# Performance work log

Measured on AMD Instinct MI355X. Metric: run time of the kernel, lower is better.

Reference implementation:

```python
import jax, jax.numpy as jnp
import numpy as np

EMBED_DIM = 512
EDGE_COUNT = 200
BATCH = 1024
N_SBJ = 1      # subject entities per example
N_OBJ = 64     # candidate object entities per example


def setup_inputs() -> dict:
    key = jax.random.key(0)
    k1, k2, k3, k4 = jax.random.split(key, 4)
    sbj_embs = jax.random.normal(k1, (BATCH, N_SBJ, EMBED_DIM), dtype=jnp.float32)
    obj_embs = jax.random.normal(k2, (BATCH, N_OBJ, EMBED_DIM), dtype=jnp.float32)
    rel_ids = jax.random.randint(k3, (BATCH,), 0, EDGE_COUNT, dtype=jnp.int64)
    # W_r initialized as diagonal matrices from uniform values (as in __init__),
    # but stored as full dense [edge_count, d, d] trainable tensor.
    diag_vals = jax.random.uniform(k4, (EDGE_COUNT, EMBED_DIM), dtype=jnp.float32)
    W_r = jax.vmap(jnp.diag)(diag_vals)  # [edge_count, d, d]
    return {"sbj_embs": sbj_embs, "obj_embs": obj_embs, "rel_ids": rel_ids, "W_r": W_r}


def reference(sbj_embs, obj_embs, rel_ids, W_r):
    # rel_embs: gather per-relation dense matrix  [B, d, d]
    rel_embs = W_r[rel_ids]
    # sbj_rel = sbj @ rel : [B, n, d]
    sbj_rel = jnp.einsum('bnd,bde->bne', sbj_embs, rel_embs)
    # scores = sbj_rel @ obj^T : [B, n, m], then sum over n -> [B, m]
    scores = jnp.einsum('bne,bme->bm', sbj_rel, obj_embs)
    return scores
```

## Files before the change

### kernel.cpp

```cpp
#include <hip/hip_runtime.h>


#define D      512
#define NOBJ   64

__global__ __launch_bounds__(256) void decoder_kernel(
    const float* __restrict__ sbj,
    const float* __restrict__ obj,
    const int*   __restrict__ rel,
    const float* __restrict__ Wr,
    float*       __restrict__ out)
{
    const int b = blockIdx.x;
    const int t = threadIdx.x;

    __shared__ float s_lds[D];
    __shared__ float v_lds[D];

    {
        const float2 sv = reinterpret_cast<const float2*>(sbj + (size_t)b * D)[t];
        s_lds[2 * t]     = sv.x;
        s_lds[2 * t + 1] = sv.y;
    }
    __syncthreads();

    const float2* __restrict__ W2 =
        reinterpret_cast<const float2*>(Wr + (size_t)rel[b] * D * D);

    float acc0 = 0.f, acc1 = 0.f;
    #pragma unroll 8
    for (int d = 0; d < D; ++d) {
        const float  sd = s_lds[d];
        const float2 w  = W2[d * (D / 2) + t];
        acc0 = fmaf(sd, w.x, acc0);
        acc1 = fmaf(sd, w.y, acc1);
    }
    v_lds[2 * t]     = acc0;
    v_lds[2 * t + 1] = acc1;
    __syncthreads();

    const int wave = t >> 6;
    const int lane = t & 63;

    float vreg[8];
    #pragma unroll
    for (int k = 0; k < 8; ++k) vreg[k] = v_lds[lane * 8 + k];

    const float* __restrict__ objb = obj + (size_t)b * NOBJ * D;

    #pragma unroll 4
    for (int j = 0; j < 16; ++j) {
        const int m = wave * 16 + j;
        const float4* __restrict__ o4 =
            reinterpret_cast<const float4*>(objb + (size_t)m * D);
        const float4 a = o4[lane * 2];
        const float4 c = o4[lane * 2 + 1];

        float p = vreg[0] * a.x + vreg[1] * a.y + vreg[2] * a.z + vreg[3] * a.w
                + vreg[4] * c.x + vreg[5] * c.y + vreg[6] * c.z + vreg[7] * c.w;

        #pragma unroll
        for (int off = 32; off > 0; off >>= 1)
            p += __shfl_down(p, off, 64);

        if (lane == 0) out[(size_t)b * NOBJ + m] = p;
    }
}

extern "C" void kernel_launch(void* const* d_in, const int* in_sizes, int n_in,
                              void* d_out, int out_size, void* d_ws, size_t ws_size,
                              hipStream_t stream) {
    const float* sbj = (const float*)d_in[0];
    const float* obj = (const float*)d_in[1];
    const int*   rel = (const int*)d_in[2];
    const float* Wr  = (const float*)d_in[3];
    float*       out = (float*)d_out;

    const int B = in_sizes[2];
    decoder_kernel<<<dim3(B), dim3(256), 0, stream>>>(sbj, obj, rel, Wr, out);
}
```

Baseline: 416.6 us.

## Group batch items by relation to reuse W_r reads across a chunk

Adds a prep kernel that bucket-sorts batch indices by relation id and splits each bucket into chunks of up to 8. A GEMV kernel then streams each relation's dense 512x512 matrix once per chunk and multiplies it against all subject vectors in that chunk, writing intermediate vectors to workspace. A separate score kernel dots those vectors with the object embeddings. This cuts redundant W_r traffic, which dominates the original per-example kernel, at the cost of two extra launches, a single-block serial prep step and a workspace round trip. It falls back to the fused kernel when the workspace is too small.

```diff
diff --git a/kernel.cpp b/kernel.cpp
--- a/kernel.cpp
+++ b/kernel.cpp
@@ -1,68 +1,199 @@
 #include <hip/hip_runtime.h>
 
 
-#define D      512
-#define NOBJ   64
-
-__global__ __launch_bounds__(256) void decoder_kernel(
-    const float* __restrict__ sbj,
-    const float* __restrict__ obj,
-    const int*   __restrict__ rel,
-    const float* __restrict__ Wr,
-    float*       __restrict__ out)
+#define D        512
+#define NOBJ     64
+#define EDGES    200
+#define G        8
+
+__device__ __forceinline__ float4 f4zero() { float4 z; z.x=z.y=z.z=z.w=0.f; return z; }
+
+__global__ __launch_bounds__(256) void prep_kernel(
+    const int* __restrict__ rel, int B,
+    int* __restrict__ sorted, int* __restrict__ chunk_rel,
+    int* __restrict__ chunk_start, int* __restrict__ chunk_cnt,
+    int* __restrict__ nchunks)
+{
+    __shared__ int cnt[EDGES];
+    __shared__ int off[EDGES];
+    __shared__ int pos[EDGES];
+    __shared__ int nch;
+    const int t = threadIdx.x;
+
+    if (t < EDGES) cnt[t] = 0;
+    if (t == 0) nch = 0;
+    __syncthreads();
+
+    for (int b = t; b < B; b += 256) atomicAdd(&cnt[rel[b]], 1);
+    __syncthreads();
+
+    if (t == 0) {
+        int a = 0;
+        for (int r = 0; r < EDGES; ++r) { off[r] = a; a += cnt[r]; }
+    }
+    if (t < EDGES) pos[t] = 0;
+    __syncthreads();
+
+    for (int b = t; b < B; b += 256) {
+        const int r = rel[b];
+        const int p = atomicAdd(&pos[r], 1);
+        sorted[off[r] + p] = b;
+    }
+
+    if (t < EDGES) {
+        const int n = cnt[t];
+        if (n > 0) {
+            const int nc   = (n + G - 1) / G;
+            const int base = atomicAdd(&nch, nc);
+            for (int k = 0; k < nc; ++k) {
+                chunk_rel[base + k]   = t;
+                chunk_start[base + k] = off[t] + k * G;
+                chunk_cnt[base + k]   = min(G, n - k * G);
+            }
+        }
+    }
+    __syncthreads();
+    if (t == 0) *nchunks = nch;
+}
+
+__global__ __launch_bounds__(256) void gemv_kernel(
+    const float* __restrict__ sbj, const float* __restrict__ Wr,
+    const int* __restrict__ sorted,
+    const int* __restrict__ chunk_rel, const int* __restrict__ chunk_start,
+    const int* __restrict__ chunk_cnt, const int* __restrict__ nchunks,
+    float* __restrict__ V)
+{
+    const int cid = blockIdx.x >> 1;
+    if (cid >= *nchunks) return;
+    const int colbase = (blockIdx.x & 1) * 256;
+    const int t    = threadIdx.x;
+    const int lane = t & 63;
+    const int wv   = t >> 6;
+
+    __shared__ float lds[8192];
+
+    const int relid = chunk_rel[cid];
+    const int start = chunk_start[cid];
+    const int cnt   = chunk_cnt[cid];
+
+    #pragma unroll
+    for (int g = 0; g < G; ++g) {
+        float2 v2;
+        if (g < cnt) {
+            v2 = reinterpret_cast<const float2*>(sbj + (size_t)sorted[start + g] * D)[t];
+        } else { v2.x = 0.f; v2.y = 0.f; }
+        lds[g * D + 2 * t]     = v2.x;
+        lds[g * D + 2 * t + 1] = v2.y;
+    }
+    __syncthreads();
+
+    const float4* __restrict__ W4 =
+        reinterpret_cast<const float4*>(Wr) + (size_t)relid * (D * D / 4) + (colbase >> 2) + lane;
+
+    float4 acc[G];
+    #pragma unroll
+    for (int g = 0; g < G; ++g) acc[g] = f4zero();
+
+    #pragma unroll 4
+    for (int d4 = 0; d4 < D; d4 += 4) {
+        const int d = d4 + wv;
+        const float4 w = W4[(size_t)d * (D / 4)];
+        #pragma unroll
+        for (int g = 0; g < G; ++g) {
+            const float sg = lds[g * D + d];
+            acc[g].x = fmaf(sg, w.x, acc[g].x);
+            acc[g].y = fmaf(sg, w.y, acc[g].y);
+            acc[g].z = fmaf(sg, w.z, acc[g].z);
+            acc[g].w = fmaf(sg, w.w, acc[g].w);
+        }
+    }
+    __syncthreads();
+
+    #pragma unroll
+    for (int g = 0; g < G; ++g)
+        reinterpret_cast<float4*>(lds)[(wv * G + g) * 64 + lane] = acc[g];
+    __syncthreads();
+
+    for (int g = 0; g < cnt; ++g) {
+        const float s = lds[(0 * G + g) * 256 + t] + lds[(1 * G + g) * 256 + t]
+                      + lds[(2 * G + g) * 256 + t] + lds[(3 * G + g) * 256 + t];
+        V[(size_t)sorted[start + g] * D + colbase + t] = s;
+    }
+}
+
+__global__ __launch_bounds__(256) void score_kernel(
+    const float* __restrict__ V, const float* __restrict__ obj,
+    float* __restrict__ out)
+{
+    const int b    = blockIdx.x;
+    const int t    = threadIdx.x;
+    const int lane = t & 63;
+    const int wv   = t >> 6;
+
+    const float4* __restrict__ v4 = reinterpret_cast<const float4*>(V + (size_t)b * D);
+    const float4 a = v4[lane * 2];
+    const float4 c = v4[lane * 2 + 1];
+    float vreg[8] = {a.x, a.y, a.z, a.w, c.x, c.y, c.z, c.w};
+
+    const float* __restrict__ objb = obj + (size_t)b * NOBJ * D;
+
+    #pragma unroll 4
+    for (int j = 0; j < 16; ++j) {
+        const int m = wv * 16 + j;
+        const float4* __restrict__ o4 = reinterpret_cast<const float4*>(objb + (size_t)m * D);
+        const float4 x = o4[lane * 2];
+        const float4 y = o4[lane * 2 + 1];
+
+        float p = vreg[0] * x.x + vreg[1] * x.y + vreg[2] * x.z + vreg[3] * x.w
+                + vreg[4] * y.x + vreg[5] * y.y + vreg[6] * y.z + vreg[7] * y.w;
+
+        #pragma unroll
+        for (int off = 32; off > 0; off >>= 1)
+            p += __shfl_down(p, off, 64);
+
+        if (lane == 0) out[(size_t)b * NOBJ + m] = p;
+    }
+}
+
+__global__ __launch_bounds__(256) void fused_kernel(
+    const float* __restrict__ sbj, const float* __restrict__ obj,
+    const int* __restrict__ rel, const float* __restrict__ Wr,
+    float* __restrict__ out)
 {
     const int b = blockIdx.x;
     const int t = threadIdx.x;
-
     __shared__ float s_lds[D];
     __shared__ float v_lds[D];
-
     {
         const float2 sv = reinterpret_cast<const float2*>(sbj + (size_t)b * D)[t];
-        s_lds[2 * t]     = sv.x;
-        s_lds[2 * t + 1] = sv.y;
-    }
-    __syncthreads();
-
-    const float2* __restrict__ W2 =
-        reinterpret_cast<const float2*>(Wr + (size_t)rel[b] * D * D);
-
+        s_lds[2 * t] = sv.x; s_lds[2 * t + 1] = sv.y;
+    }
+    __syncthreads();
+    const float2* __restrict__ W2 = reinterpret_cast<const float2*>(Wr + (size_t)rel[b] * D * D);
     float acc0 = 0.f, acc1 = 0.f;
     #pragma unroll 8
     for (int d = 0; d < D; ++d) {
-        const float  sd = s_lds[d];
-        const float2 w  = W2[d * (D / 2) + t];
-        acc0 = fmaf(sd, w.x, acc0);
-        acc1 = fmaf(sd, w.y, acc1);
-    }
-    v_lds[2 * t]     = acc0;
-    v_lds[2 * t + 1] = acc1;
-    __syncthreads();
-
-    const int wave = t >> 6;
-    const int lane = t & 63;
-
+        const float sd = s_lds[d];
+        const float2 w = W2[d * (D / 2) + t];
+        acc0 = fmaf(sd, w.x, acc0); acc1 = fmaf(sd, w.y, acc1);
+    }
+    v_lds[2 * t] = acc0; v_lds[2 * t + 1] = acc1;
+    __syncthreads();
+    const int wave = t >> 6, lane = t & 63;
     float vreg[8];
     #pragma unroll
     for (int k = 0; k < 8; ++k) vreg[k] = v_lds[lane * 8 + k];
-
     const float* __restrict__ objb = obj + (size_t)b * NOBJ * D;
-
     #pragma unroll 4
     for (int j = 0; j < 16; ++j) {
         const int m = wave * 16 + j;
-        const float4* __restrict__ o4 =
-            reinterpret_cast<const float4*>(objb + (size_t)m * D);
+        const float4* __restrict__ o4 = reinterpret_cast<const float4*>(objb + (size_t)m * D);
         const float4 a = o4[lane * 2];
         const float4 c = o4[lane * 2 + 1];
-
-        float p = vreg[0] * a.x + vreg[1] * a.y + vreg[2] * a.z + vreg[3] * a.w
-                + vreg[4] * c.x + vreg[5] * c.y + vreg[6] * c.z + vreg[7] * c.w;
-
+        float p = vreg[0]*a.x + vreg[1]*a.y + vreg[2]*a.z + vreg[3]*a.w
+                + vreg[4]*c.x + vreg[5]*c.y + vreg[6]*c.z + vreg[7]*c.w;
         #pragma unroll
-        for (int off = 32; off > 0; off >>= 1)
-            p += __shfl_down(p, off, 64);
-
+        for (int off = 32; off > 0; off >>= 1) p += __shfl_down(p, off, 64);
         if (lane == 0) out[(size_t)b * NOBJ + m] = p;
     }
 }
@@ -75,7 +206,35 @@
     const int*   rel = (const int*)d_in[2];
     const float* Wr  = (const float*)d_in[3];
     float*       out = (float*)d_out;
-
     const int B = in_sizes[2];
-    decoder_kernel<<<dim3(B), dim3(256), 0, stream>>>(sbj, obj, rel, Wr, out);
-}
+
+    const int maxch = B / G + EDGES;
+
+    const size_t offV      = 0;
+    const size_t offSorted = (size_t)B * D * 4;
+    const size_t offCRel   = offSorted + (size_t)B * 4;
+    const size_t offCStart = offCRel   + (size_t)maxch * 4;
+    const size_t offCCnt   = offCStart + (size_t)maxch * 4;
+    const size_t offNCh    = offCCnt   + (size_t)maxch * 4;
+    const size_t needed    = offNCh + 64;
+
+    if (ws_size < needed) {
+        fused_kernel<<<dim3(B), dim3(256), 0, stream>>>(sbj, obj, rel, Wr, out);
+        return;
+    }
+
+    char* ws = (char*)d_ws;
+    float* V          = (float*)(ws + offV);
+    int*   sorted     = (int*)(ws + offSorted);
+    int*   chunk_rel  = (int*)(ws + offCRel);
+    int*   chunk_start= (int*)(ws + offCStart);
+    int*   chunk_cnt  = (int*)(ws + offCCnt);
+    int*   nchunks    = (int*)(ws + offNCh);
+
+    prep_kernel<<<dim3(1), dim3(256), 0, stream>>>(rel, B, sorted, chunk_rel,
+                                                   chunk_start, chunk_cnt, nchunks);
+    gemv_kernel<<<dim3(2 * maxch), dim3(256), 0, stream>>>(sbj, Wr, sorted,
+                                                           chunk_rel, chunk_start,
+                                                           chunk_cnt, nchunks, V);
+    score_kernel<<<dim3(B), dim3(256), 0, stream>>>(V, obj, out);
+}
```

Result: faster. 382.8 us (-8.1%).

## Sort batch by relation and map same-relation blocks to one XCD for L2 reuse

Applied to the files above, without the earlier changes.

Adds a single-block prep kernel that counting-sorts batch indices by relation id into workspace. The main kernel remaps block ids so that consecutive sorted examples land on the same XCD, letting blocks that share a W_r matrix reuse it from that XCD's L2 instead of refetching the 1 MB matrix from HBM. The W-times-s product is also restructured into two halves of d using float4 loads, reduced through LDS. This costs an extra serial launch and a single-block sort, and the original kernel is kept as a fallback when workspace is too small.

```diff
diff --git a/kernel.cpp b/kernel.cpp
--- a/kernel.cpp
+++ b/kernel.cpp
@@ -3,19 +3,60 @@
 
 #define D      512
 #define NOBJ   64
+#define EDGES  200
 
-__global__ __launch_bounds__(256) void decoder_kernel(
-    const float* __restrict__ sbj,
-    const float* __restrict__ obj,
-    const int*   __restrict__ rel,
-    const float* __restrict__ Wr,
-    float*       __restrict__ out)
+__global__ __launch_bounds__(256) void prep_kernel(
+    const int* __restrict__ rel, int B, int* __restrict__ sorted)
 {
-    const int b = blockIdx.x;
+    __shared__ int cnt[256];
+    __shared__ int scan[256];
+    __shared__ int off[256];
+    __shared__ int pos[256];
     const int t = threadIdx.x;
 
+    cnt[t] = 0; pos[t] = 0;
+    __syncthreads();
+
+    for (int b = t; b < B; b += 256) atomicAdd(&cnt[rel[b]], 1);
+    __syncthreads();
+
+    int val = cnt[t];
+    scan[t] = val;
+    __syncthreads();
+    for (int o = 1; o < 256; o <<= 1) {
+        int v = (t >= o) ? scan[t - o] : 0;
+        __syncthreads();
+        scan[t] += v;
+        __syncthreads();
+    }
+    off[t] = scan[t] - val;
+    __syncthreads();
+
+    for (int b = t; b < B; b += 256) {
+        const int r = rel[b];
+        sorted[off[r] + atomicAdd(&pos[r], 1)] = b;
+    }
+}
+
+__global__ __launch_bounds__(256) void main_kernel(
+    const float* __restrict__ sbj, const float* __restrict__ obj,
+    const float* __restrict__ Wr,  const int* __restrict__ rel,
+    const int* __restrict__ sorted, float* __restrict__ out)
+{
+    int wg;
+    {
+        const int nwg = gridDim.x;
+        const int q = nwg >> 3, r = nwg & 7;
+        const int xcd = blockIdx.x & 7, idx = blockIdx.x >> 3;
+        wg = (xcd < r ? xcd * (q + 1) : r * (q + 1) + (xcd - r) * q) + idx;
+    }
+    const int b    = sorted[wg];
+    const int t    = threadIdx.x;
+    const int lane = t & 63;
+    const int wv   = t >> 6;
+
     __shared__ float s_lds[D];
-    __shared__ float v_lds[D];
+    __shared__ float p_lds[2 * D];
 
     {
         const float2 sv = reinterpret_cast<const float2*>(sbj + (size_t)b * D)[t];
@@ -24,33 +65,53 @@
     }
     __syncthreads();
 
-    const float2* __restrict__ W2 =
-        reinterpret_cast<const float2*>(Wr + (size_t)rel[b] * D * D);
+    const int c4 = (t & 127) << 2;
+    const int h  = t >> 7;
 
-    float acc0 = 0.f, acc1 = 0.f;
-    #pragma unroll 8
-    for (int d = 0; d < D; ++d) {
-        const float  sd = s_lds[d];
-        const float2 w  = W2[d * (D / 2) + t];
-        acc0 = fmaf(sd, w.x, acc0);
-        acc1 = fmaf(sd, w.y, acc1);
+    const float4* __restrict__ W4 =
+        reinterpret_cast<const float4*>(Wr + (size_t)rel[b] * D * D)
+        + (size_t)(h * 256) * (D / 4) + (c4 >> 2);
+    const float* __restrict__ sp = s_lds + h * 256;
+
+    float4 acc; acc.x = acc.y = acc.z = acc.w = 0.f;
+
+    #pragma unroll 4
+    for (int d4 = 0; d4 < 256; d4 += 4) {
+        const float4 sd4 = *reinterpret_cast<const float4*>(sp + d4);
+        const float4 w0 = W4[(size_t)(d4 + 0) * (D / 4)];
+        const float4 w1 = W4[(size_t)(d4 + 1) * (D / 4)];
+        const float4 w2 = W4[(size_t)(d4 + 2) * (D / 4)];
+        const float4 w3 = W4[(size_t)(d4 + 3) * (D / 4)];
+        acc.x = fmaf(sd4.x, w0.x, acc.x); acc.y = fmaf(sd4.x, w0.y, acc.y);
+        acc.z = fmaf(sd4.x, w0.z, acc.z); acc.w = fmaf(sd4.x, w0.w, acc.w);
+        acc.x = fmaf(sd4.y, w1.x, acc.x); acc.y = fmaf(sd4.y, w1.y, acc.y);
+        acc.z = fmaf(sd4.y, w1.z, acc.z); acc.w = fmaf(sd4.y, w1.w, acc.w);
+        acc.x = fmaf(sd4.z, w2.x, acc.x); acc.y = fmaf(sd4.z, w2.y, acc.y);
+        acc.z = fmaf(sd4.z, w2.z, acc.z); acc.w = fmaf(sd4.z, w2.w, acc.w);
+        acc.x = fmaf(sd4.w, w3.x, acc.x); acc.y = fmaf(sd4.w, w3.y, acc.y);
+        acc.z = fmaf(sd4.w, w3.z, acc.z); acc.w = fmaf(sd4.w, w3.w, acc.w);
     }
-    v_lds[2 * t]     = acc0;
-    v_lds[2 * t + 1] = acc1;
+
+    reinterpret_cast<float4*>(p_lds)[h * 128 + (c4 >> 2)] = acc;
     __syncthreads();
 
-    const int wave = t >> 6;
-    const int lane = t & 63;
+    {
+        const float2 pa = *reinterpret_cast<const float2*>(p_lds + 2 * t);
+        const float2 pb = *reinterpret_cast<const float2*>(p_lds + D + 2 * t);
+        s_lds[2 * t]     = pa.x + pb.x;
+        s_lds[2 * t + 1] = pa.y + pb.y;
+    }
+    __syncthreads();
 
     float vreg[8];
     #pragma unroll
-    for (int k = 0; k < 8; ++k) vreg[k] = v_lds[lane * 8 + k];
+    for (int k = 0; k < 8; ++k) vreg[k] = s_lds[lane * 8 + k];
 
     const float* __restrict__ objb = obj + (size_t)b * NOBJ * D;
 
     #pragma unroll 4
     for (int j = 0; j < 16; ++j) {
-        const int m = wave * 16 + j;
+        const int m = wv * 16 + j;
         const float4* __restrict__ o4 =
             reinterpret_cast<const float4*>(objb + (size_t)m * D);
         const float4 a = o4[lane * 2];
@@ -67,6 +128,49 @@
     }
 }
 
+__global__ __launch_bounds__(256) void fused_kernel(
+    const float* __restrict__ sbj, const float* __restrict__ obj,
+    const int* __restrict__ rel, const float* __restrict__ Wr,
+    float* __restrict__ out)
+{
+    const int b = blockIdx.x;
+    const int t = threadIdx.x;
+    __shared__ float s_lds[D];
+    __shared__ float v_lds[D];
+    {
+        const float2 sv = reinterpret_cast<const float2*>(sbj + (size_t)b * D)[t];
+        s_lds[2 * t] = sv.x; s_lds[2 * t + 1] = sv.y;
+    }
+    __syncthreads();
+    const float2* __restrict__ W2 = reinterpret_cast<const float2*>(Wr + (size_t)rel[b] * D * D);
+    float acc0 = 0.f, acc1 = 0.f;
+    #pragma unroll 8
+    for (int d = 0; d < D; ++d) {
+        const float sd = s_lds[d];
+        const float2 w = W2[d * (D / 2) + t];
+        acc0 = fmaf(sd, w.x, acc0); acc1 = fmaf(sd, w.y, acc1);
+    }
+    v_lds[2 * t] = acc0; v_lds[2 * t + 1] = acc1;
+    __syncthreads();
+    const int wave = t >> 6, lane = t & 63;
+    float vreg[8];
+    #pragma unroll
+    for (int k = 0; k < 8; ++k) vreg[k] = v_lds[lane * 8 + k];
+    const float* __restrict__ objb = obj + (size_t)b * NOBJ * D;
+    #pragma unroll 4
+    for (int j = 0; j < 16; ++j) {
+        const int mm = wave * 16 + j;
+        const float4* __restrict__ o4 = reinterpret_cast<const float4*>(objb + (size_t)mm * D);
+        const float4 a = o4[lane * 2];
+        const float4 c = o4[lane * 2 + 1];
+        float p = vreg[0]*a.x + vreg[1]*a.y + vreg[2]*a.z + vreg[3]*a.w
+                + vreg[4]*c.x + vreg[5]*c.y + vreg[6]*c.z + vreg[7]*c.w;
+        #pragma unroll
+        for (int off = 32; off > 0; off >>= 1) p += __shfl_down(p, off, 64);
+        if (lane == 0) out[(size_t)b * NOBJ + mm] = p;
+    }
+}
+
 extern "C" void kernel_launch(void* const* d_in, const int* in_sizes, int n_in,
                               void* d_out, int out_size, void* d_ws, size_t ws_size,
                               hipStream_t stream) {
@@ -75,7 +179,14 @@
     const int*   rel = (const int*)d_in[2];
     const float* Wr  = (const float*)d_in[3];
     float*       out = (float*)d_out;
+    const int B = in_sizes[2];
 
-    const int B = in_sizes[2];
-    decoder_kernel<<<dim3(B), dim3(256), 0, stream>>>(sbj, obj, rel, Wr, out);
+    if (ws_size < (size_t)B * 4) {
+        fused_kernel<<<dim3(B), dim3(256), 0, stream>>>(sbj, obj, rel, Wr, out);
+        return;
+    }
+
+    int* sorted = (int*)d_ws;
+    prep_kernel<<<dim3(1), dim3(256), 0, stream>>>(rel, B, sorted);
+    main_kernel<<<dim3(B), dim3(256), 0, stream>>>(sbj, obj, Wr, rel, sorted, out);
 }
```

New measurement: 390.2 us. -6.3%, faster.
